# Kernel tuning notes

Hardware: AMD Instinct MI355X
Metric: run time of the kernel (lower is better)

The kernel has to match this reference:

```python
import jax, jax.numpy as jnp
import numpy as np

BS, N, H = 8, 2048, 512
NEG_INF = -1.0e9
LEAKY_SLOPE = 0.01  # torch nn.LeakyReLU default


def setup_inputs() -> dict:
    key = jax.random.key(0)
    ks = jax.random.split(key, 8)
    feats = jax.random.normal(ks[0], (BS, N, H), dtype=jnp.float32)
    # random 0/1 adjacency with self-loops so every row has >=1 neighbor
    adj = jax.random.randint(ks[1], (BS, N, N), 0, 2).astype(jnp.float32)
    adj = jnp.maximum(adj, jnp.eye(N, dtype=jnp.float32)[None])
    s = 1.0 / np.sqrt(H)
    return {
        "feats": feats,
        "adj_mat": adj,
        "fc_w": jax.random.normal(ks[2], (H, H), dtype=jnp.float32) * s,
        "fc_b": jax.random.normal(ks[3], (H,), dtype=jnp.float32) * s,
        "q_w": jax.random.normal(ks[4], (1, H), dtype=jnp.float32) * s,
        "q_b": jax.random.normal(ks[5], (1,), dtype=jnp.float32) * s,
        "k_w": jax.random.normal(ks[6], (1, H), dtype=jnp.float32) * s,
        "k_b": jax.random.normal(ks[7], (1,), dtype=jnp.float32) * s,
    }


def reference(feats, adj_mat, fc_w, fc_b, q_w, q_b, k_w, k_b):
    # feats: [bs, N, H]; torch Linear: x @ W.T + b
    feat_proj = jnp.einsum("bnh,oh->bno", feats, fc_w) + fc_b          # [bs, N, H]
    q = jnp.einsum("bnh,oh->bno", feat_proj, q_w) + q_b                # [bs, N, 1]
    k = jnp.einsum("bnh,oh->bno", feat_proj, k_w) + k_b                # [bs, N, 1]
    logits = q + jnp.swapaxes(k, 2, 1)                                 # [bs, N, N] broadcast add
    masked = logits + (1.0 - adj_mat) * NEG_INF
    masked = jnp.where(masked >= 0, masked, LEAKY_SLOPE * masked)      # LeakyReLU
    atten = jax.nn.softmax(masked, axis=-1)
    # dropout is identity in eval mode
    out = jnp.einsum("bnm,bmh->bnh", atten, feat_proj)
    return out + feats  # residual=True
```

## Files before the change

kernel.cpp:

```cpp
#include <hip/hip_runtime.h>
#include <hip/hip_bf16.h>
#include <cstdint>
#include <cstddef>

#define BSZ 8
#define NN 2048
#define HH 512
#define MROWS (BSZ * NN)

typedef __attribute__((ext_vector_type(4))) float f32x4;
typedef __attribute__((ext_vector_type(8))) short short8;
typedef __attribute__((ext_vector_type(4))) unsigned short us4;

static __device__ __forceinline__ unsigned short f2bf(float f) {
    uint32_t u = __builtin_bit_cast(uint32_t, f);
    u += 0x7fffu + ((u >> 16) & 1u);
    return (unsigned short)(u >> 16);
}

static __device__ __forceinline__ void async16(const unsigned short* g, unsigned short* l) {
    __builtin_amdgcn_global_load_lds(
        (const __attribute__((address_space(1))) void*)g,
        (__attribute__((address_space(3))) void*)l, 16, 0, 0);
}

__global__ __launch_bounds__(256) void k1_kernel(
    const float* __restrict__ feats, const float* __restrict__ fc_w,
    const float* __restrict__ fc_b, const float* __restrict__ q_w,
    const float* __restrict__ k_w, const float* __restrict__ adj,
    unsigned short* __restrict__ fpT, unsigned char* __restrict__ maskb,
    float* __restrict__ qpart, float* __restrict__ kpart) {
    const int bid = blockIdx.x;
    const int tid = threadIdx.x;
    if (bid < 512) {
        __shared__ alignas(16) unsigned short As[128 * 32];
        __shared__ alignas(16) unsigned short Bs[128 * 32];
        __shared__ float qred[2][128], kred[2][128];
        const int wave = tid >> 6, lane = tid & 63;
        const int wi = wave >> 1, wj = wave & 1;
        const int n0 = (bid & 3) * 128;
        const int i0 = (bid >> 2) * 128;
        const int r0 = tid >> 3;
        const int c4 = (tid & 7) * 4;
        const int fro = (lane & 15) * 32 + (lane >> 4) * 8;
        f32x4 acc[4][4];
#pragma unroll
        for (int a = 0; a < 4; ++a)
#pragma unroll
            for (int c = 0; c < 4; ++c) acc[a][c] = (f32x4)(0.f);

        for (int k0 = 0; k0 < HH; k0 += 32) {
            __syncthreads();
#pragma unroll
            for (int m = 0; m < 4; ++m) {
                f32x4 av = *(const f32x4*)&feats[(size_t)(i0 + r0 + 32 * m) * HH + k0 + c4];
                f32x4 bv = *(const f32x4*)&fc_w[(size_t)(n0 + r0 + 32 * m) * HH + k0 + c4];
                us4 oa, ob;
#pragma unroll
                for (int c = 0; c < 4; ++c) { oa[c] = f2bf(av[c]); ob[c] = f2bf(bv[c]); }
                *(us4*)&As[(r0 + 32 * m) * 32 + c4] = oa;
                *(us4*)&Bs[(r0 + 32 * m) * 32 + c4] = ob;
            }
            __syncthreads();
            short8 af[4], bf[4];
#pragma unroll
            for (int t = 0; t < 4; ++t) af[t] = *(const short8*)&As[(wi * 64 + t * 16) * 32 + fro];
#pragma unroll
            for (int t = 0; t < 4; ++t) bf[t] = *(const short8*)&Bs[(wj * 64 + t * 16) * 32 + fro];
#pragma unroll
            for (int it = 0; it < 4; ++it)
#pragma unroll
                for (int jt = 0; jt < 4; ++jt)
                    acc[it][jt] = __builtin_amdgcn_mfma_f32_16x16x32_bf16(af[it], bf[jt], acc[it][jt], 0, 0, 0);
        }

        int colv[4]; float cbv[4], qwv[4], kwv[4];
#pragma unroll
        for (int jt = 0; jt < 4; ++jt) {
            colv[jt] = n0 + wj * 64 + jt * 16 + (lane & 15);
            cbv[jt] = fc_b[colv[jt]];
            qwv[jt] = q_w[colv[jt]];
            kwv[jt] = k_w[colv[jt]];
        }
        const int b = i0 >> 11;
        const int il = i0 & 2047;
#pragma unroll
        for (int jt = 0; jt < 4; ++jt) {
#pragma unroll
            for (int it = 0; it < 4; ++it) {
                const int rb = wi * 64 + it * 16 + ((lane >> 4) << 2);
                us4 o;
#pragma unroll
                for (int r = 0; r < 4; ++r) o[r] = f2bf(acc[it][jt][r] + cbv[jt]);
                *(us4*)(fpT + ((size_t)b * HH + colv[jt]) * NN + il + rb) = o;
            }
        }
#pragma unroll
        for (int it = 0; it < 4; ++it) {
#pragma unroll
            for (int r = 0; r < 4; ++r) {
                float pq = 0.f, pk = 0.f;
#pragma unroll
                for (int jt = 0; jt < 4; ++jt) {
                    float v = acc[it][jt][r] + cbv[jt];
                    pq += v * qwv[jt];
                    pk += v * kwv[jt];
                }
                for (int off = 1; off < 16; off <<= 1) {
                    pq += __shfl_xor(pq, off, 64);
                    pk += __shfl_xor(pk, off, 64);
                }
                if ((lane & 15) == 0) {
                    const int rr = wi * 64 + it * 16 + ((lane >> 4) << 2) + r;
                    qred[wj][rr] = pq;
                    kred[wj][rr] = pk;
                }
            }
        }
        __syncthreads();
        if (tid < 128) {
            const size_t o = (size_t)(n0 >> 7) * MROWS + i0 + tid;
            qpart[o] = qred[0][tid] + qred[1][tid];
            kpart[o] = kred[0][tid] + kred[1][tid];
        }
    } else {
        const int a = bid - 512;
        const int wave = tid >> 6, lane = tid & 63;
#pragma unroll
        for (int s = 0; s < 4; ++s) {
            const int row = a * 16 + s * 4 + wave;
            const float* ar = adj + (size_t)row * NN;
#pragma unroll
            for (int p = 0; p < 4; ++p) {
                f32x4 v0 = *(const f32x4*)&ar[p * 512 + lane * 8];
                f32x4 v1 = *(const f32x4*)&ar[p * 512 + lane * 8 + 4];
                float fb = v0[0] + 2.f * v0[1] + 4.f * v0[2] + 8.f * v0[3]
                         + 16.f * v1[0] + 32.f * v1[1] + 64.f * v1[2] + 128.f * v1[3];
                maskb[(size_t)row * 256 + p * 64 + lane] = (unsigned char)(unsigned int)fb;
            }
        }
    }
}

__global__ __launch_bounds__(256) void fused_pv_kernel(
    const unsigned short* __restrict__ fpT, const unsigned char* __restrict__ maskb,
    const float* __restrict__ qpart, const float* __restrict__ kpart,
    const float* __restrict__ q_b, const float* __restrict__ k_b,
    const float* __restrict__ feats, float* __restrict__ out) {
    __shared__ alignas(16) unsigned short As[128 * 32];
    __shared__ alignas(16) unsigned short Bs[128 * 32];
    __shared__ float kLDS[NN];
    __shared__ float qLDS[128];
    __shared__ float zbuf[4][32][8];
    __shared__ float rzl[128];
    const int tid = threadIdx.x;
    const int wave = tid >> 6, lane = tid & 63;
    const int wi = wave >> 1, wj = wave & 1;
    const int bid = blockIdx.x;
    const int b = bid & 7;
    const int t6 = bid >> 3;
    const int i0 = (t6 >> 2) * 128;
    const int n0 = (t6 & 3) * 128;
    const size_t rowbase = (size_t)b * NN + i0;

    {
        const float kb = k_b[0], qb = q_b[0];
#pragma unroll
        for (int s = 0; s < 8; ++s) {
            const int j = s * 256 + tid;
            const size_t gj = (size_t)b * NN + j;
            kLDS[j] = qpart[0] * 0.f + kpart[gj] + kpart[MROWS + gj]
                    + kpart[2 * MROWS + gj] + kpart[3 * MROWS + gj] + kb;
        }
        if (tid < 128) {
            const size_t gi = rowbase + tid;
            qLDS[tid] = qpart[gi] + qpart[MROWS + gi]
                      + qpart[2 * MROWS + gi] + qpart[3 * MROWS + gi] + qb;
        }
    }
    __syncthreads();

    const int r0 = tid >> 3;
    const int c4 = (tid & 7) * 4;
    float qi[4];
#pragma unroll
    for (int m = 0; m < 4; ++m) qi[m] = qLDS[r0 + 32 * m];
    float z[4] = {0.f, 0.f, 0.f, 0.f};

    const unsigned short* Bt = fpT + (size_t)b * HH * NN;
    const uint32_t* mk = (const uint32_t*)maskb;
    const int lrow = lane >> 2, lseg = (lane & 3) * 8;
    const int fro = (lane & 15) * 32 + (lane >> 4) * 8;

    f32x4 acc[4][4];
#pragma unroll
    for (int a = 0; a < 4; ++a)
#pragma unroll
        for (int c = 0; c < 4; ++c) acc[a][c] = (f32x4)(0.f);

    uint32_t mcur[4];
#pragma unroll
    for (int m = 0; m < 4; ++m) mcur[m] = mk[(rowbase + r0 + 32 * m) * 64];

    for (int k0 = 0; k0 < NN; k0 += 32) {
        __syncthreads();
        {
            const int c0 = wave * 2;
            const unsigned short* gb = Bt + (size_t)(n0 + c0 * 16 + lrow) * NN + k0 + lseg;
            async16(gb, &Bs[(c0 * 16) * 32]);
            async16(gb + (size_t)16 * NN, &Bs[(c0 * 16 + 16) * 32]);
        }
        uint32_t mnext[4];
        if (k0 + 32 < NN) {
#pragma unroll
            for (int m = 0; m < 4; ++m)
                mnext[m] = mk[(rowbase + r0 + 32 * m) * 64 + ((k0 + 32) >> 5)];
        }
        const f32x4 kv = *(const f32x4*)&kLDS[k0 + c4];
#pragma unroll
        for (int m = 0; m < 4; ++m) {
            const uint32_t nib = (mcur[m] >> c4) & 0xFu;
            us4 o;
#pragma unroll
            for (int c = 0; c < 4; ++c) {
                float s = qi[m] + kv[c];
                s = (s >= 0.f) ? s : 0.01f * s;
                const float e = __expf(s);
                const float wv = ((nib >> c) & 1u) ? e : 0.f;
                z[m] += wv;
                o[c] = f2bf(wv);
            }
            *(us4*)&As[(r0 + 32 * m) * 32 + c4] = o;
        }
        __syncthreads();
        short8 af[4], bf[4];
#pragma unroll
        for (int t = 0; t < 4; ++t) af[t] = *(const short8*)&As[(wi * 64 + t * 16) * 32 + fro];
#pragma unroll
        for (int t = 0; t < 4; ++t) bf[t] = *(const short8*)&Bs[(wj * 64 + t * 16) * 32 + fro];
#pragma unroll
        for (int it = 0; it < 4; ++it)
#pragma unroll
            for (int jt = 0; jt < 4; ++jt)
                acc[it][jt] = __builtin_amdgcn_mfma_f32_16x16x32_bf16(af[it], bf[jt], acc[it][jt], 0, 0, 0);
#pragma unroll
        for (int m = 0; m < 4; ++m) mcur[m] = mnext[m];
    }

#pragma unroll
    for (int m = 0; m < 4; ++m) zbuf[m][r0][tid & 7] = z[m];
    __syncthreads();
    if (tid < 128) {
        float s = 0.f;
        const float* zp = zbuf[tid >> 5][tid & 31];
#pragma unroll
        for (int j = 0; j < 8; ++j) s += zp[j];
        rzl[tid] = 1.0f / s;
    }
    __syncthreads();

#pragma unroll
    for (int it = 0; it < 4; ++it) {
        const int rb = wi * 64 + it * 16 + ((lane >> 4) << 2);
        float rv[4];
#pragma unroll
        for (int r = 0; r < 4; ++r) rv[r] = rzl[rb + r];
#pragma unroll
        for (int jt = 0; jt < 4; ++jt) {
            const int col = n0 + wj * 64 + jt * 16 + (lane & 15);
#pragma unroll
            for (int r = 0; r < 4; ++r) {
                const size_t idx = (rowbase + rb + r) * HH + col;
                out[idx] = acc[it][jt][r] * rv[r] + feats[idx];
            }
        }
    }
}

extern "C" void kernel_launch(void* const* d_in, const int* in_sizes, int n_in,
                              void* d_out, int out_size, void* d_ws, size_t ws_size,
                              hipStream_t stream) {
    const float* feats = (const float*)d_in[0];
    const float* adj   = (const float*)d_in[1];
    const float* fc_w  = (const float*)d_in[2];
    const float* fc_b  = (const float*)d_in[3];
    const float* q_w   = (const float*)d_in[4];
    const float* q_b   = (const float*)d_in[5];
    const float* k_w   = (const float*)d_in[6];
    const float* k_b   = (const float*)d_in[7];
    float* out = (float*)d_out;

    char* w = (char*)d_ws;
    auto alloc = [&](size_t bytes) {
        char* p = w;
        w += (bytes + 255) & ~(size_t)255;
        return p;
    };
    unsigned short* fpT   = (unsigned short*)alloc((size_t)BSZ * HH * NN * 2);
    unsigned char*  maskb = (unsigned char*)alloc((size_t)MROWS * 256);
    float* qpart = (float*)alloc((size_t)4 * MROWS * 4);
    float* kpart = (float*)alloc((size_t)4 * MROWS * 4);

    k1_kernel<<<512 + 1024, 256, 0, stream>>>(feats, fc_w, fc_b, q_w, k_w, adj,
                                              fpT, maskb, qpart, kpart);
    fused_pv_kernel<<<BSZ * (NN / 128) * (HH / 128), 256, 0, stream>>>(
        fpT, maskb, qpart, kpart, q_b, k_b, feats, out);
}
```

Baseline: 337.4 us.

## Retile fused attention-PV kernel to 64x256 tiles with cheaper exp and bf16 packing

Changes the fused kernel's output tile from 128x128 to 64 rows by 256 columns. Each block now computes softmax weights for only 64 rows, which halves the redundant exp work repeated across column tiles, but it loads twice as much fpT per block. The logits are pre-scaled by log2(e) so a native exp2 can be used, LeakyReLU becomes fmax, and the bf16 conversion changes to round-half-up with a perm-based pack. Register use for the accumulators is unchanged, and the grid stays at 512 blocks.

```diff
diff --git a/kernel.cpp b/kernel.cpp
--- a/kernel.cpp
+++ b/kernel.cpp
@@ -7,10 +7,18 @@
 #define NN 2048
 #define HH 512
 #define MROWS (BSZ * NN)
+#define LOG2E 1.44269504088896f
 
 typedef __attribute__((ext_vector_type(4))) float f32x4;
 typedef __attribute__((ext_vector_type(8))) short short8;
 typedef __attribute__((ext_vector_type(4))) unsigned short us4;
+typedef __attribute__((ext_vector_type(4))) uint32_t u32x4;
+
+#if __has_builtin(__builtin_amdgcn_exp2f)
+#define EXP2(x) __builtin_amdgcn_exp2f(x)
+#else
+#define EXP2(x) __expf((x) * 0.69314718056f)
+#endif
 
 static __device__ __forceinline__ unsigned short f2bf(float f) {
     uint32_t u = __builtin_bit_cast(uint32_t, f);
@@ -147,20 +155,20 @@
     const float* __restrict__ qpart, const float* __restrict__ kpart,
     const float* __restrict__ q_b, const float* __restrict__ k_b,
     const float* __restrict__ feats, float* __restrict__ out) {
-    __shared__ alignas(16) unsigned short As[128 * 32];
-    __shared__ alignas(16) unsigned short Bs[128 * 32];
+    __shared__ alignas(16) unsigned short As[64 * 32];
+    __shared__ alignas(16) unsigned short Bs[256 * 32];
     __shared__ float kLDS[NN];
-    __shared__ float qLDS[128];
-    __shared__ float zbuf[4][32][8];
-    __shared__ float rzl[128];
+    __shared__ float qLDS[64];
+    __shared__ float zfl[256];
+    __shared__ float rzl[64];
     const int tid = threadIdx.x;
     const int wave = tid >> 6, lane = tid & 63;
     const int wi = wave >> 1, wj = wave & 1;
     const int bid = blockIdx.x;
     const int b = bid & 7;
     const int t6 = bid >> 3;
-    const int i0 = (t6 >> 2) * 128;
-    const int n0 = (t6 & 3) * 128;
+    const int i0 = (t6 >> 1) * 64;
+    const int n0 = (t6 & 1) * 256;
     const size_t rowbase = (size_t)b * NN + i0;
 
     {
@@ -169,105 +177,98 @@
         for (int s = 0; s < 8; ++s) {
             const int j = s * 256 + tid;
             const size_t gj = (size_t)b * NN + j;
-            kLDS[j] = qpart[0] * 0.f + kpart[gj] + kpart[MROWS + gj]
-                    + kpart[2 * MROWS + gj] + kpart[3 * MROWS + gj] + kb;
-        }
-        if (tid < 128) {
+            kLDS[j] = (kpart[gj] + kpart[MROWS + gj] + kpart[2 * MROWS + gj]
+                     + kpart[3 * MROWS + gj] + kb) * LOG2E;
+        }
+        if (tid < 64) {
             const size_t gi = rowbase + tid;
-            qLDS[tid] = qpart[gi] + qpart[MROWS + gi]
-                      + qpart[2 * MROWS + gi] + qpart[3 * MROWS + gi] + qb;
+            qLDS[tid] = (qpart[gi] + qpart[MROWS + gi] + qpart[2 * MROWS + gi]
+                       + qpart[3 * MROWS + gi] + qb) * LOG2E;
         }
     }
     __syncthreads();
 
-    const int r0 = tid >> 3;
-    const int c4 = (tid & 7) * 4;
-    float qi[4];
-#pragma unroll
-    for (int m = 0; m < 4; ++m) qi[m] = qLDS[r0 + 32 * m];
-    float z[4] = {0.f, 0.f, 0.f, 0.f};
+    const int r0 = tid >> 2;
+    const int c8 = (tid & 3) * 8;
+    const float qi = qLDS[r0];
+    float z = 0.f;
 
     const unsigned short* Bt = fpT + (size_t)b * HH * NN;
     const uint32_t* mk = (const uint32_t*)maskb;
+    const size_t mrow = (rowbase + r0) * 64;
     const int lrow = lane >> 2, lseg = (lane & 3) * 8;
     const int fro = (lane & 15) * 32 + (lane >> 4) * 8;
 
-    f32x4 acc[4][4];
-#pragma unroll
-    for (int a = 0; a < 4; ++a)
-#pragma unroll
-        for (int c = 0; c < 4; ++c) acc[a][c] = (f32x4)(0.f);
-
-    uint32_t mcur[4];
-#pragma unroll
-    for (int m = 0; m < 4; ++m) mcur[m] = mk[(rowbase + r0 + 32 * m) * 64];
-
+    f32x4 acc[2][8];
+#pragma unroll
+    for (int a = 0; a < 2; ++a)
+#pragma unroll
+        for (int c = 0; c < 8; ++c) acc[a][c] = (f32x4)(0.f);
+
+    uint32_t mcur = mk[mrow];
     for (int k0 = 0; k0 < NN; k0 += 32) {
         __syncthreads();
         {
-            const int c0 = wave * 2;
-            const unsigned short* gb = Bt + (size_t)(n0 + c0 * 16 + lrow) * NN + k0 + lseg;
-            async16(gb, &Bs[(c0 * 16) * 32]);
-            async16(gb + (size_t)16 * NN, &Bs[(c0 * 16 + 16) * 32]);
-        }
-        uint32_t mnext[4];
-        if (k0 + 32 < NN) {
-#pragma unroll
-            for (int m = 0; m < 4; ++m)
-                mnext[m] = mk[(rowbase + r0 + 32 * m) * 64 + ((k0 + 32) >> 5)];
-        }
-        const f32x4 kv = *(const f32x4*)&kLDS[k0 + c4];
-#pragma unroll
-        for (int m = 0; m < 4; ++m) {
-            const uint32_t nib = (mcur[m] >> c4) & 0xFu;
-            us4 o;
-#pragma unroll
-            for (int c = 0; c < 4; ++c) {
-                float s = qi[m] + kv[c];
-                s = (s >= 0.f) ? s : 0.01f * s;
-                const float e = __expf(s);
-                const float wv = ((nib >> c) & 1u) ? e : 0.f;
-                z[m] += wv;
-                o[c] = f2bf(wv);
-            }
-            *(us4*)&As[(r0 + 32 * m) * 32 + c4] = o;
-        }
+            const int rbase = wave * 64;
+            const unsigned short* gb = Bt + (size_t)(n0 + rbase + lrow) * NN + k0 + lseg;
+            async16(gb, &Bs[rbase * 32]);
+            async16(gb + (size_t)16 * NN, &Bs[(rbase + 16) * 32]);
+            async16(gb + (size_t)32 * NN, &Bs[(rbase + 32) * 32]);
+            async16(gb + (size_t)48 * NN, &Bs[(rbase + 48) * 32]);
+        }
+        uint32_t mnext = 0;
+        if (k0 + 32 < NN) mnext = mk[mrow + ((k0 + 32) >> 5)];
+        const f32x4 kv0 = *(const f32x4*)&kLDS[k0 + c8];
+        const f32x4 kv1 = *(const f32x4*)&kLDS[k0 + c8 + 4];
+        const uint32_t byte8 = (mcur >> c8) & 0xffu;
+        float wv[8];
+#pragma unroll
+        for (int c = 0; c < 8; ++c) {
+            float s = qi + (c < 4 ? kv0[c] : kv1[c - 4]);
+            s = fmaxf(s, 0.01f * s);
+            float e = EXP2(s);
+            wv[c] = ((byte8 >> c) & 1u) ? e : 0.f;
+            z += wv[c];
+        }
+        u32x4 pk;
+#pragma unroll
+        for (int p = 0; p < 4; ++p) {
+            uint32_t lo = __builtin_bit_cast(uint32_t, wv[2 * p]) + 0x8000u;
+            uint32_t hi = __builtin_bit_cast(uint32_t, wv[2 * p + 1]) + 0x8000u;
+            pk[p] = __builtin_amdgcn_perm(hi, lo, 0x07060302u);
+        }
+        *(u32x4*)&As[r0 * 32 + c8] = pk;
         __syncthreads();
-        short8 af[4], bf[4];
-#pragma unroll
-        for (int t = 0; t < 4; ++t) af[t] = *(const short8*)&As[(wi * 64 + t * 16) * 32 + fro];
-#pragma unroll
-        for (int t = 0; t < 4; ++t) bf[t] = *(const short8*)&Bs[(wj * 64 + t * 16) * 32 + fro];
-#pragma unroll
-        for (int it = 0; it < 4; ++it)
-#pragma unroll
-            for (int jt = 0; jt < 4; ++jt)
+        short8 af[2], bf[8];
+#pragma unroll
+        for (int t = 0; t < 2; ++t) af[t] = *(const short8*)&As[(wi * 32 + t * 16) * 32 + fro];
+#pragma unroll
+        for (int t = 0; t < 8; ++t) bf[t] = *(const short8*)&Bs[(wj * 128 + t * 16) * 32 + fro];
+#pragma unroll
+        for (int it = 0; it < 2; ++it)
+#pragma unroll
+            for (int jt = 0; jt < 8; ++jt)
                 acc[it][jt] = __builtin_amdgcn_mfma_f32_16x16x32_bf16(af[it], bf[jt], acc[it][jt], 0, 0, 0);
-#pragma unroll
-        for (int m = 0; m < 4; ++m) mcur[m] = mnext[m];
-    }
-
-#pragma unroll
-    for (int m = 0; m < 4; ++m) zbuf[m][r0][tid & 7] = z[m];
+        mcur = mnext;
+    }
+
+    zfl[tid] = z;
     __syncthreads();
-    if (tid < 128) {
-        float s = 0.f;
-        const float* zp = zbuf[tid >> 5][tid & 31];
-#pragma unroll
-        for (int j = 0; j < 8; ++j) s += zp[j];
-        rzl[tid] = 1.0f / s;
+    if (tid < 64) {
+        const float* zp = &zfl[tid * 4];
+        rzl[tid] = 1.0f / (zp[0] + zp[1] + zp[2] + zp[3]);
     }
     __syncthreads();
 
 #pragma unroll
-    for (int it = 0; it < 4; ++it) {
-        const int rb = wi * 64 + it * 16 + ((lane >> 4) << 2);
+    for (int it = 0; it < 2; ++it) {
+        const int rb = wi * 32 + it * 16 + ((lane >> 4) << 2);
         float rv[4];
 #pragma unroll
         for (int r = 0; r < 4; ++r) rv[r] = rzl[rb + r];
 #pragma unroll
-        for (int jt = 0; jt < 4; ++jt) {
-            const int col = n0 + wj * 64 + jt * 16 + (lane & 15);
+        for (int jt = 0; jt < 8; ++jt) {
+            const int col = n0 + wj * 128 + jt * 16 + (lane & 15);
 #pragma unroll
             for (int r = 0; r < 4; ++r) {
                 const size_t idx = (rowbase + rb + r) * HH + col;
@@ -303,6 +304,6 @@
 
     k1_kernel<<<512 + 1024, 256, 0, stream>>>(feats, fc_w, fc_b, q_w, k_w, adj,
                                               fpT, maskb, qpart, kpart);
-    fused_pv_kernel<<<BSZ * (NN / 128) * (HH / 128), 256, 0, stream>>>(
+    fused_pv_kernel<<<512, 256, 0, stream>>>(
         fpT, maskb, qpart, kpart, q_b, k_b, feats, out);
 }
```

After: 320.1 us. -5.1%, faster.
